# Optimization experiments

Hardware: AMD Instinct MI355X
Metric: run time of the kernel (lower is better)

Reference implementation:

```python
import jax, jax.numpy as jnp
import numpy as np

B, T, C, W, H, HID = 64, 1024, 256, 28, 28, 512


def setup_inputs() -> dict:
    key = jax.random.key(0)
    k1, k2, k3, k4, k5, k6 = jax.random.split(key, 6)
    text = jax.random.normal(k1, (B, T), dtype=jnp.float32)
    vision = jax.random.normal(k2, (B, C, W, H), dtype=jnp.float32)
    s1 = 1.0 / np.sqrt(T + C)
    s2 = 1.0 / np.sqrt(HID)
    W1 = jax.random.uniform(k3, (T + C, HID), jnp.float32, -s1, s1)
    b1 = jax.random.uniform(k4, (HID,), jnp.float32, -s1, s1)
    W2 = jax.random.uniform(k5, (HID, 1), jnp.float32, -s2, s2)
    b2 = jax.random.uniform(k6, (1,), jnp.float32, -s2, s2)
    return {"text": text, "vision": vision, "W1": W1, "b1": b1, "W2": W2, "b2": b2}


def reference(text, vision, W1, b1, W2, b2):
    b, c, w, h = vision.shape
    p = w * h
    # pixels in (i*height + j) order, matching the torch double loop / view
    pixels = vision.transpose(0, 2, 3, 1).reshape(b, p, c)  # (B, P, C)
    text_b = jnp.broadcast_to(text[:, None, :], (b, p, text.shape[1]))
    feat = jnp.concatenate([text_b, pixels], axis=-1)        # (B, P, T+C)
    hidden = jax.nn.relu(jnp.einsum("bpf,fh->bph", feat, W1) + b1)
    scores = (jnp.einsum("bph,ho->bpo", hidden, W2) + b2)[..., 0]  # (B, P)
    weights = jax.nn.softmax(scores, axis=1)                 # (B, P)
    pooled = jnp.einsum("bpc,bp->bc", pixels, weights)       # (B, C)
    return jnp.concatenate([pooled, text], axis=1)           # (B, C+T)
```

## Files before the change

### kernel.cpp

```cpp
#include <hip/hip_runtime.h>

#define BB  64
#define TT  1024
#define CC  256
#define PP  784
#define HID 512
#define FF  1280

typedef float v4f __attribute__((ext_vector_type(4)));
typedef short v8s __attribute__((ext_vector_type(8)));

__device__ inline unsigned int bf16_rne_bits(float x) {
    unsigned int u = __float_as_uint(x);
    unsigned int r = u + 0x7FFFu + ((u >> 16) & 1u);
    return r & 0xFFFF0000u;
}

__global__ __launch_bounds__(256) void k_w1t(const float* __restrict__ W1,
                                             unsigned short* __restrict__ w1t_hi,
                                             unsigned short* __restrict__ w1t_lo) {
    const int id = blockIdx.x * 256 + threadIdx.x;
    const int h  = id & 511;
    const int cg = id >> 9;
    const int cstep = cg >> 2, g = cg & 3;
    const float* W1v = W1 + (size_t)TT * HID;
    unsigned int hw[4], lw[4];
    #pragma unroll
    for (int k = 0; k < 4; ++k) {
        const int c0 = cstep * 32 + g * 8 + 2 * k;
        float x0 = W1v[(size_t)c0 * HID + h];
        float x1 = W1v[(size_t)(c0 + 1) * HID + h];
        unsigned int h0 = bf16_rne_bits(x0), h1 = bf16_rne_bits(x1);
        unsigned int l0 = bf16_rne_bits(x0 - __uint_as_float(h0));
        unsigned int l1 = bf16_rne_bits(x1 - __uint_as_float(h1));
        hw[k] = (h0 >> 16) | (h1 & 0xFFFF0000u);
        lw[k] = (l0 >> 16) | (l1 & 0xFFFF0000u);
    }
    const size_t eoff = ((size_t)((h >> 8) * 8 + cstep) * 256 + (h & 255)) * 32 + g * 8;
    *(int4*)(&w1t_hi[eoff]) = make_int4(hw[0], hw[1], hw[2], hw[3]);
    *(int4*)(&w1t_lo[eoff]) = make_int4(lw[0], lw[1], lw[2], lw[3]);
}

__global__ __launch_bounds__(512) void k_text_gemm(const float* __restrict__ text,
                                                   const float* __restrict__ W1,
                                                   float* __restrict__ tbp) {
    const int b  = blockIdx.x;
    const int ks = blockIdx.y;
    const int t  = threadIdx.x;
    __shared__ float st[128];
    if (t < 128) st[t] = text[b * TT + ks * 128 + t];
    __syncthreads();
    float acc = 0.f;
    const float* wp = W1 + (size_t)(ks * 128) * HID + t;
    #pragma unroll 4
    for (int k = 0; k < 128; ++k)
        acc = fmaf(st[k], wp[(size_t)k * HID], acc);
    tbp[(b * 8 + ks) * HID + t] = acc;
}

__global__ __launch_bounds__(256, 2) void k_vision_mfma(
        const float* __restrict__ vision,
        const unsigned short* __restrict__ w1t_hi,
        const unsigned short* __restrict__ w1t_lo,
        const float* __restrict__ b1,
        const float* __restrict__ W2,
        const float* __restrict__ tbp,
        float* __restrict__ scores) {
    const int ptile = blockIdx.x;
    const int hh    = blockIdx.y;
    const int b     = blockIdx.z;
    const int tid   = threadIdx.x;
    const int lane  = tid & 63;
    const int w     = tid >> 6;
    const int l15   = lane & 15, lg = lane >> 4;

    __shared__ int4 lds4[2][896];

    v4f acc[7][4];
    #pragma unroll
    for (int m = 0; m < 7; ++m)
        #pragma unroll
        for (int n = 0; n < 4; ++n) acc[m][n] = (v4f){0.f, 0.f, 0.f, 0.f};

    const size_t vbase = (size_t)b * (CC * PP) + ptile * 112;
    const int spx = tid >> 1, sch = tid & 1;

    float xv[16];
    #define A_LOAD(KS) do { if (tid < 224) { \
        _Pragma("unroll") for (int j = 0; j < 16; ++j) { \
            const int c_ = (KS) * 32 + sch * 16 + j; \
            xv[j] = vision[vbase + (size_t)c_ * PP + spx]; } } } while (0)

    #define A_WRITE(BUF) do { if (tid < 224) { \
        unsigned int hw[8], lw[8]; \
        _Pragma("unroll") for (int q = 0; q < 8; ++q) { \
            unsigned int h0 = bf16_rne_bits(xv[2 * q]); \
            unsigned int h1 = bf16_rne_bits(xv[2 * q + 1]); \
            unsigned int l0 = bf16_rne_bits(xv[2 * q] - __uint_as_float(h0)); \
            unsigned int l1 = bf16_rne_bits(xv[2 * q + 1] - __uint_as_float(h1)); \
            hw[q] = (h0 >> 16) | (h1 & 0xFFFF0000u); \
            lw[q] = (l0 >> 16) | (l1 & 0xFFFF0000u); } \
        int4* ah = (int4*)(&lds4[BUF][0]) + (spx * 4 + sch * 2); \
        int4* al = (int4*)((char*)&lds4[BUF][0] + 7168) + (spx * 4 + sch * 2); \
        ah[0] = make_int4(hw[0], hw[1], hw[2], hw[3]); \
        ah[1] = make_int4(hw[4], hw[5], hw[6], hw[7]); \
        al[0] = make_int4(lw[0], lw[1], lw[2], lw[3]); \
        al[1] = make_int4(lw[4], lw[5], lw[6], lw[7]); } } while (0)

    A_LOAD(0);
    A_WRITE(0);
    __syncthreads();

    const int bfr = ((w * 64 + l15) * 4 + lg) * 8;

    for (int ks = 0; ks < 8; ++ks) {
        const int cur = ks & 1;
        if (ks < 7) A_LOAD(ks + 1);
        const unsigned short* bkh = w1t_hi + (size_t)(hh * 8 + ks) * 8192 + bfr;
        const unsigned short* bkl = w1t_lo + (size_t)(hh * 8 + ks) * 8192 + bfr;
        v8s bh[4], bl[4];
        #pragma unroll
        for (int n = 0; n < 4; ++n) {
            bh[n] = *(const v8s*)(bkh + n * 512);
            bl[n] = *(const v8s*)(bkl + n * 512);
        }
        const char* abuf = (const char*)&lds4[cur][0];
        #pragma unroll
        for (int m = 0; m < 7; ++m) {
            const int fo = ((m * 16 + l15) * 4 + lg) * 16;
            const v8s ah = *(const v8s*)(abuf + fo);
            const v8s al = *(const v8s*)(abuf + 7168 + fo);
            #pragma unroll
            for (int n = 0; n < 4; ++n) {
                acc[m][n] = __builtin_amdgcn_mfma_f32_16x16x32_bf16(ah, bh[n], acc[m][n], 0, 0, 0);
                acc[m][n] = __builtin_amdgcn_mfma_f32_16x16x32_bf16(ah, bl[n], acc[m][n], 0, 0, 0);
                acc[m][n] = __builtin_amdgcn_mfma_f32_16x16x32_bf16(al, bh[n], acc[m][n], 0, 0, 0);
            }
        }
        if (ks < 7) A_WRITE(cur ^ 1);
        __syncthreads();
    }

    float tbn[4], w2n[4];
    #pragma unroll
    for (int n = 0; n < 4; ++n) {
        const int hglob = hh * 256 + w * 64 + n * 16 + l15;
        const float* tp = tbp + (size_t)b * 8 * HID + hglob;
        float tv = b1[hglob];
        #pragma unroll
        for (int q = 0; q < 8; ++q) tv += tp[q * HID];
        tbn[n] = tv;
        w2n[n] = W2[hglob];
    }
    const int px0 = ptile * 112 + lg * 4;
    #pragma unroll
    for (int m = 0; m < 7; ++m) {
        #pragma unroll
        for (int r = 0; r < 4; ++r) {
            float s = 0.f;
            #pragma unroll
            for (int n = 0; n < 4; ++n)
                s += fmaxf(acc[m][n][r] + tbn[n], 0.f) * w2n[n];
            s += __shfl_xor(s, 1, 64);
            s += __shfl_xor(s, 2, 64);
            s += __shfl_xor(s, 4, 64);
            s += __shfl_xor(s, 8, 64);
            if (l15 == 0)
                atomicAdd(&scores[b * PP + px0 + m * 16 + r], s);
        }
    }
    #undef A_LOAD
    #undef A_WRITE
}

__global__ __launch_bounds__(256) void k_softmax_copy(float* __restrict__ sw,
                                                      const float* __restrict__ text,
                                                      float* __restrict__ out) {
    const int b   = blockIdx.x;
    const int tid = threadIdx.x;
    const int lane = tid & 63, wid = tid >> 6;
    __shared__ float red[4];

    float v[4]; int cnt = 0;
    float m = -3.4e38f;
    for (int p = tid; p < PP; p += 256) { v[cnt] = sw[b * PP + p]; m = fmaxf(m, v[cnt]); ++cnt; }
    #pragma unroll
    for (int off = 32; off > 0; off >>= 1) m = fmaxf(m, __shfl_xor(m, off, 64));
    if (lane == 0) red[wid] = m;
    __syncthreads();
    m = fmaxf(fmaxf(red[0], red[1]), fmaxf(red[2], red[3]));
    __syncthreads();

    float ssum = 0.f;
    for (int i = 0; i < cnt; ++i) { v[i] = expf(v[i] - m); ssum += v[i]; }
    #pragma unroll
    for (int off = 32; off > 0; off >>= 1) ssum += __shfl_xor(ssum, off, 64);
    if (lane == 0) red[wid] = ssum;
    __syncthreads();
    const float inv = 1.f / (red[0] + red[1] + red[2] + red[3]);

    cnt = 0;
    for (int p = tid; p < PP; p += 256) sw[b * PP + p] = v[cnt++] * inv;

    for (int j = tid; j < TT; j += 256) out[b * FF + CC + j] = text[b * TT + j];
}

__global__ __launch_bounds__(256) void k_pool(const float* __restrict__ vision,
                                              const float* __restrict__ wts,
                                              float* __restrict__ out) {
    const int cg = blockIdx.x;
    const int b  = blockIdx.y;
    const int tid = threadIdx.x, lane = tid & 63, wid = tid >> 6;
    __shared__ float wl[PP];
    {
        const int i = tid * 4;
        if (i < PP) *(float4*)&wl[i] = *(const float4*)&wts[b * PP + i];
    }
    __syncthreads();
    #pragma unroll
    for (int ci = 0; ci < 8; ++ci) {
        const int c = cg * 32 + wid * 8 + ci;
        const float* vr = vision + (size_t)b * (CC * PP) + (size_t)c * PP;
        float acc = 0.f;
        #pragma unroll
        for (int k = 0; k < 4; ++k) {
            const int p4 = (lane + 64 * k) * 4;
            if (p4 < PP) {
                const float4 vv = *(const float4*)(vr + p4);
                const float4 ww = *(const float4*)&wl[p4];
                acc = fmaf(vv.x, ww.x, acc);
                acc = fmaf(vv.y, ww.y, acc);
                acc = fmaf(vv.z, ww.z, acc);
                acc = fmaf(vv.w, ww.w, acc);
            }
        }
        #pragma unroll
        for (int off = 32; off > 0; off >>= 1) acc += __shfl_xor(acc, off, 64);
        if (lane == 0) out[b * FF + c] = acc;
    }
}

extern "C" void kernel_launch(void* const* d_in, const int* in_sizes, int n_in,
                              void* d_out, int out_size, void* d_ws, size_t ws_size,
                              hipStream_t stream) {
    const float* text   = (const float*)d_in[0];
    const float* vision = (const float*)d_in[1];
    const float* W1     = (const float*)d_in[2];
    const float* b1     = (const float*)d_in[3];
    const float* W2     = (const float*)d_in[4];
    float* out = (float*)d_out;

    float* tbp = (float*)d_ws;
    float* sw  = tbp + BB * 8 * HID;
    unsigned short* w1t_hi = (unsigned short*)(sw + BB * PP);
    unsigned short* w1t_lo = w1t_hi + 131072;

    k_w1t        <<<64, 256, 0, stream>>>(W1, w1t_hi, w1t_lo);
    k_text_gemm  <<<dim3(BB, 8), 512, 0, stream>>>(text, W1, tbp);
    hipMemsetAsync(sw, 0, BB * PP * sizeof(float), stream);
    k_vision_mfma<<<dim3(7, 2, BB), 256, 0, stream>>>(vision, w1t_hi, w1t_lo,
                                                      b1, W2, tbp, sw);
    k_softmax_copy<<<BB, 256, 0, stream>>>(sw, text, out);
    k_pool       <<<dim3(8, BB), 256, 0, stream>>>(vision, sw, out);
}
```

Before: 175.0 us.

## Use 1024-thread blocks covering all hidden units, reducing scores in LDS

The vision GEMM kernel now uses 1024-thread blocks, each spanning all 512 hidden units for a 112-pixel tile, instead of two 256-thread blocks per tile. Each vision tile is therefore loaded and split into bf16 only once. Per-wave partial scores are summed in shared memory and written directly, which removes the global atomics and the memset. The k-loop is unrolled by two with register double-buffering and lighter LDS-only barriers, and the W1 repack layout is simplified to match the new B-fragment indexing. The cost is a larger block, fewer accumulators per wave, and the risk of lower occupancy from the 1024-thread launch bounds.

```diff
diff --git a/kernel.cpp b/kernel.cpp
--- a/kernel.cpp
+++ b/kernel.cpp
@@ -16,18 +16,23 @@
     return r & 0xFFFF0000u;
 }
 
+__device__ inline void barrier_lds_only() {
+    asm volatile("s_waitcnt lgkmcnt(0)" ::: "memory");
+    __builtin_amdgcn_s_barrier();
+}
+
 __global__ __launch_bounds__(256) void k_w1t(const float* __restrict__ W1,
                                              unsigned short* __restrict__ w1t_hi,
                                              unsigned short* __restrict__ w1t_lo) {
     const int id = blockIdx.x * 256 + threadIdx.x;
-    const int h  = id & 511;
-    const int cg = id >> 9;
-    const int cstep = cg >> 2, g = cg & 3;
+    const int ks = id >> 11;
+    const int h  = (id >> 2) & 511;
+    const int g  = id & 3;
     const float* W1v = W1 + (size_t)TT * HID;
     unsigned int hw[4], lw[4];
     #pragma unroll
     for (int k = 0; k < 4; ++k) {
-        const int c0 = cstep * 32 + g * 8 + 2 * k;
+        const int c0 = ks * 32 + g * 8 + 2 * k;
         float x0 = W1v[(size_t)c0 * HID + h];
         float x1 = W1v[(size_t)(c0 + 1) * HID + h];
         unsigned int h0 = bf16_rne_bits(x0), h1 = bf16_rne_bits(x1);
@@ -36,9 +41,8 @@
         hw[k] = (h0 >> 16) | (h1 & 0xFFFF0000u);
         lw[k] = (l0 >> 16) | (l1 & 0xFFFF0000u);
     }
-    const size_t eoff = ((size_t)((h >> 8) * 8 + cstep) * 256 + (h & 255)) * 32 + g * 8;
-    *(int4*)(&w1t_hi[eoff]) = make_int4(hw[0], hw[1], hw[2], hw[3]);
-    *(int4*)(&w1t_lo[eoff]) = make_int4(lw[0], lw[1], lw[2], lw[3]);
+    *(int4*)(&w1t_hi[(size_t)id * 8]) = make_int4(hw[0], hw[1], hw[2], hw[3]);
+    *(int4*)(&w1t_lo[(size_t)id * 8]) = make_int4(lw[0], lw[1], lw[2], lw[3]);
 }
 
 __global__ __launch_bounds__(512) void k_text_gemm(const float* __restrict__ text,
@@ -58,7 +62,7 @@
     tbp[(b * 8 + ks) * HID + t] = acc;
 }
 
-__global__ __launch_bounds__(256, 2) void k_vision_mfma(
+__global__ __launch_bounds__(1024, 4) void k_vision_mfma(
         const float* __restrict__ vision,
         const unsigned short* __restrict__ w1t_hi,
         const unsigned short* __restrict__ w1t_lo,
@@ -67,110 +71,127 @@
         const float* __restrict__ tbp,
         float* __restrict__ scores) {
     const int ptile = blockIdx.x;
-    const int hh    = blockIdx.y;
-    const int b     = blockIdx.z;
+    const int b     = blockIdx.y;
     const int tid   = threadIdx.x;
     const int lane  = tid & 63;
     const int w     = tid >> 6;
     const int l15   = lane & 15, lg = lane >> 4;
 
-    __shared__ int4 lds4[2][896];
-
-    v4f acc[7][4];
-    #pragma unroll
-    for (int m = 0; m < 7; ++m)
-        #pragma unroll
-        for (int n = 0; n < 4; ++n) acc[m][n] = (v4f){0.f, 0.f, 0.f, 0.f};
+    __shared__ char albuf[2][14336];
+    __shared__ float sred[16 * 112];
+
+    v4f acc[7][2];
+    #pragma unroll
+    for (int m = 0; m < 7; ++m) {
+        acc[m][0] = (v4f){0.f, 0.f, 0.f, 0.f};
+        acc[m][1] = (v4f){0.f, 0.f, 0.f, 0.f};
+    }
 
     const size_t vbase = (size_t)b * (CC * PP) + ptile * 112;
-    const int spx = tid >> 1, sch = tid & 1;
-
-    float xv[16];
-    #define A_LOAD(KS) do { if (tid < 224) { \
-        _Pragma("unroll") for (int j = 0; j < 16; ++j) { \
-            const int c_ = (KS) * 32 + sch * 16 + j; \
-            xv[j] = vision[vbase + (size_t)c_ * PP + spx]; } } } while (0)
-
-    #define A_WRITE(BUF) do { if (tid < 224) { \
-        unsigned int hw[8], lw[8]; \
-        _Pragma("unroll") for (int q = 0; q < 8; ++q) { \
-            unsigned int h0 = bf16_rne_bits(xv[2 * q]); \
-            unsigned int h1 = bf16_rne_bits(xv[2 * q + 1]); \
-            unsigned int l0 = bf16_rne_bits(xv[2 * q] - __uint_as_float(h0)); \
-            unsigned int l1 = bf16_rne_bits(xv[2 * q + 1] - __uint_as_float(h1)); \
-            hw[q] = (h0 >> 16) | (h1 & 0xFFFF0000u); \
-            lw[q] = (l0 >> 16) | (l1 & 0xFFFF0000u); } \
-        int4* ah = (int4*)(&lds4[BUF][0]) + (spx * 4 + sch * 2); \
-        int4* al = (int4*)((char*)&lds4[BUF][0] + 7168) + (spx * 4 + sch * 2); \
-        ah[0] = make_int4(hw[0], hw[1], hw[2], hw[3]); \
-        ah[1] = make_int4(hw[4], hw[5], hw[6], hw[7]); \
-        al[0] = make_int4(lw[0], lw[1], lw[2], lw[3]); \
-        al[1] = make_int4(lw[4], lw[5], lw[6], lw[7]); } } while (0)
-
-    A_LOAD(0);
-    A_WRITE(0);
-    __syncthreads();
-
-    const int bfr = ((w * 64 + l15) * 4 + lg) * 8;
-
-    for (int ks = 0; ks < 8; ++ks) {
-        const int cur = ks & 1;
-        if (ks < 7) A_LOAD(ks + 1);
-        const unsigned short* bkh = w1t_hi + (size_t)(hh * 8 + ks) * 8192 + bfr;
-        const unsigned short* bkl = w1t_lo + (size_t)(hh * 8 + ks) * 8192 + bfr;
-        v8s bh[4], bl[4];
-        #pragma unroll
-        for (int n = 0; n < 4; ++n) {
-            bh[n] = *(const v8s*)(bkh + n * 512);
-            bl[n] = *(const v8s*)(bkl + n * 512);
-        }
-        const char* abuf = (const char*)&lds4[cur][0];
-        #pragma unroll
-        for (int m = 0; m < 7; ++m) {
-            const int fo = ((m * 16 + l15) * 4 + lg) * 16;
-            const v8s ah = *(const v8s*)(abuf + fo);
-            const v8s al = *(const v8s*)(abuf + 7168 + fo);
-            #pragma unroll
-            for (int n = 0; n < 4; ++n) {
-                acc[m][n] = __builtin_amdgcn_mfma_f32_16x16x32_bf16(ah, bh[n], acc[m][n], 0, 0, 0);
-                acc[m][n] = __builtin_amdgcn_mfma_f32_16x16x32_bf16(ah, bl[n], acc[m][n], 0, 0, 0);
-                acc[m][n] = __builtin_amdgcn_mfma_f32_16x16x32_bf16(al, bh[n], acc[m][n], 0, 0, 0);
-            }
-        }
-        if (ks < 7) A_WRITE(cur ^ 1);
-        __syncthreads();
-    }
-
-    float tbn[4], w2n[4];
-    #pragma unroll
-    for (int n = 0; n < 4; ++n) {
-        const int hglob = hh * 256 + w * 64 + n * 16 + l15;
-        const float* tp = tbp + (size_t)b * 8 * HID + hglob;
-        float tv = b1[hglob];
+    const int spx = tid >> 3;
+    const int scg = tid & 7;
+    const bool stg = (tid < 896);
+
+    float xa[4], xb[4];
+
+    #define A_LOAD(XV, KS) do { \
+        _Pragma("unroll") for (int j = 0; j < 4; ++j) { \
+            const int c_ = (KS) * 32 + scg * 4 + j; \
+            XV[j] = vision[vbase + (size_t)c_ * PP + spx]; } } while (0)
+
+    #define A_WRITE(BUF, XV) do { \
+        unsigned int h0_ = bf16_rne_bits(XV[0]); \
+        unsigned int h1_ = bf16_rne_bits(XV[1]); \
+        unsigned int h2_ = bf16_rne_bits(XV[2]); \
+        unsigned int h3_ = bf16_rne_bits(XV[3]); \
+        unsigned int l0_ = bf16_rne_bits(XV[0] - __uint_as_float(h0_)); \
+        unsigned int l1_ = bf16_rne_bits(XV[1] - __uint_as_float(h1_)); \
+        unsigned int l2_ = bf16_rne_bits(XV[2] - __uint_as_float(h2_)); \
+        unsigned int l3_ = bf16_rne_bits(XV[3] - __uint_as_float(h3_)); \
+        int2 hp_ = make_int2((h0_ >> 16) | (h1_ & 0xFFFF0000u), \
+                             (h2_ >> 16) | (h3_ & 0xFFFF0000u)); \
+        int2 lp_ = make_int2((l0_ >> 16) | (l1_ & 0xFFFF0000u), \
+                             (l2_ >> 16) | (l3_ & 0xFFFF0000u)); \
+        *(int2*)(&albuf[BUF][spx * 64 + scg * 8])        = hp_; \
+        *(int2*)(&albuf[BUF][7168 + spx * 64 + scg * 8]) = lp_; } while (0)
+
+    const int bfr = ((w * 32 + l15) * 4 + lg) * 8;
+
+    #define COMPUTE(KS, BUF) do { \
+        const unsigned short* bph_ = w1t_hi + (size_t)(KS) * 16384 + bfr; \
+        const unsigned short* bpl_ = w1t_lo + (size_t)(KS) * 16384 + bfr; \
+        const v8s bh0 = *(const v8s*)(bph_); \
+        const v8s bh1 = *(const v8s*)(bph_ + 512); \
+        const v8s bl0 = *(const v8s*)(bpl_); \
+        const v8s bl1 = *(const v8s*)(bpl_ + 512); \
+        const char* ab_ = &albuf[BUF][0]; \
+        v8s ahr[7]; \
+        _Pragma("unroll") for (int m = 0; m < 7; ++m) \
+            ahr[m] = *(const v8s*)(ab_ + (m * 16 + l15) * 64 + lg * 16); \
+        _Pragma("unroll") for (int m = 0; m < 7; ++m) \
+            acc[m][0] = __builtin_amdgcn_mfma_f32_16x16x32_bf16(ahr[m], bh0, acc[m][0], 0, 0, 0); \
+        _Pragma("unroll") for (int m = 0; m < 7; ++m) \
+            acc[m][1] = __builtin_amdgcn_mfma_f32_16x16x32_bf16(ahr[m], bh1, acc[m][1], 0, 0, 0); \
+        _Pragma("unroll") for (int m = 0; m < 7; ++m) \
+            acc[m][0] = __builtin_amdgcn_mfma_f32_16x16x32_bf16(ahr[m], bl0, acc[m][0], 0, 0, 0); \
+        _Pragma("unroll") for (int m = 0; m < 7; ++m) \
+            acc[m][1] = __builtin_amdgcn_mfma_f32_16x16x32_bf16(ahr[m], bl1, acc[m][1], 0, 0, 0); \
+        _Pragma("unroll") for (int m = 0; m < 7; ++m) { \
+            const v8s alr = *(const v8s*)(ab_ + 7168 + (m * 16 + l15) * 64 + lg * 16); \
+            acc[m][0] = __builtin_amdgcn_mfma_f32_16x16x32_bf16(alr, bh0, acc[m][0], 0, 0, 0); \
+            acc[m][1] = __builtin_amdgcn_mfma_f32_16x16x32_bf16(alr, bh1, acc[m][1], 0, 0, 0); \
+        } } while (0)
+
+    if (stg) { A_LOAD(xa, 0); A_LOAD(xb, 1); A_WRITE(0, xa); }
+    barrier_lds_only();
+
+    for (int s = 0; s < 8; s += 2) {
+        if (stg && s + 2 < 8) A_LOAD(xa, s + 2);
+        COMPUTE(s, 0);
+        if (stg) A_WRITE(1, xb);
+        barrier_lds_only();
+        if (stg && s + 3 < 8) A_LOAD(xb, s + 3);
+        COMPUTE(s + 1, 1);
+        if (stg && s + 2 < 8) A_WRITE(0, xa);
+        barrier_lds_only();
+    }
+
+    float tbn[2], w2n[2];
+    #pragma unroll
+    for (int nn = 0; nn < 2; ++nn) {
+        const int h = w * 32 + nn * 16 + l15;
+        const float* tp = tbp + (size_t)b * 8 * HID + h;
+        float tv = b1[h];
         #pragma unroll
         for (int q = 0; q < 8; ++q) tv += tp[q * HID];
-        tbn[n] = tv;
-        w2n[n] = W2[hglob];
-    }
-    const int px0 = ptile * 112 + lg * 4;
+        tbn[nn] = tv;
+        w2n[nn] = W2[h];
+    }
     #pragma unroll
     for (int m = 0; m < 7; ++m) {
         #pragma unroll
         for (int r = 0; r < 4; ++r) {
             float s = 0.f;
             #pragma unroll
-            for (int n = 0; n < 4; ++n)
-                s += fmaxf(acc[m][n][r] + tbn[n], 0.f) * w2n[n];
+            for (int nn = 0; nn < 2; ++nn)
+                s += fmaxf(acc[m][nn][r] + tbn[nn], 0.f) * w2n[nn];
             s += __shfl_xor(s, 1, 64);
             s += __shfl_xor(s, 2, 64);
             s += __shfl_xor(s, 4, 64);
             s += __shfl_xor(s, 8, 64);
-            if (l15 == 0)
-                atomicAdd(&scores[b * PP + px0 + m * 16 + r], s);
+            if (l15 == 0) sred[w * 112 + m * 16 + lg * 4 + r] = s;
         }
+    }
+    __syncthreads();
+    if (tid < 112) {
+        float s = 0.f;
+        #pragma unroll
+        for (int q = 0; q < 16; ++q) s += sred[q * 112 + tid];
+        scores[b * PP + ptile * 112 + tid] = s;
     }
     #undef A_LOAD
     #undef A_WRITE
+    #undef COMPUTE
 }
 
 __global__ __launch_bounds__(256) void k_softmax_copy(float* __restrict__ sw,
@@ -257,9 +278,8 @@
 
     k_w1t        <<<64, 256, 0, stream>>>(W1, w1t_hi, w1t_lo);
     k_text_gemm  <<<dim3(BB, 8), 512, 0, stream>>>(text, W1, tbp);
-    hipMemsetAsync(sw, 0, BB * PP * sizeof(float), stream);
-    k_vision_mfma<<<dim3(7, 2, BB), 256, 0, stream>>>(vision, w1t_hi, w1t_lo,
-                                                      b1, W2, tbp, sw);
+    k_vision_mfma<<<dim3(7, BB), 1024, 0, stream>>>(vision, w1t_hi, w1t_lo,
+                                                    b1, W2, tbp, sw);
     k_softmax_copy<<<BB, 256, 0, stream>>>(sw, text, out);
     k_pool       <<<dim3(8, BB), 256, 0, stream>>>(vision, sw, out);
 }
```

New measurement: 191.7 us. +9.5%, slower.
